# Optimization experiments

Measured on AMD Instinct MI355X. Metric: run time of the kernel, lower is better.

Reference implementation:

```python
import jax, jax.numpy as jnp
import numpy as np

NA, NS = 50000, 5000          # artist / style node counts
E_AA, E_AS = 500000, 250000   # edges per edge type
C, ED = 128, 8                # hidden dim, edge-attr dim
DIN_A, DIN_S = 128, 64        # input feature dims
NUM_LAYERS = 3


def _l2norm(x):
    # F.normalize(x, dim=-1): x / max(||x||_2, eps)
    n = jnp.sqrt(jnp.sum(x * x, axis=-1, keepdims=True))
    return x / jnp.maximum(n, 1e-12)


def _gatv2(x_src, x_dst, src, dst, eattr, Wl, Wr, att, We, b, num_dst):
    # PyG GATv2Conv, heads=1, concat=True, add_self_loops=False, edge_dim=ED
    xl = x_src @ Wl                      # [Nsrc, C] transformed source
    xr = x_dst @ Wr                      # [Ndst, C] transformed target
    m = xl[src] + xr[dst] + eattr @ We   # [E, C]
    e = jax.nn.leaky_relu(m, 0.2) @ att  # [E] attention logits
    # segment softmax over destination nodes
    emax = jax.ops.segment_max(e, dst, num_segments=num_dst)
    ee = jnp.exp(e - emax[dst])
    den = jax.ops.segment_sum(ee, dst, num_segments=num_dst)
    alpha = ee / jnp.maximum(den[dst], 1e-16)
    out = jax.ops.segment_sum(alpha[:, None] * xl[src], dst, num_segments=num_dst)
    return out + b


def setup_inputs() -> dict:
    key = jax.random.key(0)
    ks = iter(jax.random.split(key, 40))
    r = lambda shape, s=1.0: s * jax.random.normal(next(ks), shape, dtype=jnp.float32)
    d = {}
    d['x_artist'] = r((NA, DIN_A))
    d['x_style'] = r((NS, DIN_S))
    d['src_aa'] = jax.random.randint(next(ks), (E_AA,), 0, NA, dtype=jnp.int32)
    d['dst_aa'] = jax.random.randint(next(ks), (E_AA,), 0, NA, dtype=jnp.int32)
    d['eattr_aa'] = r((E_AA, ED))
    d['src_as'] = jax.random.randint(next(ks), (E_AS,), 0, NA, dtype=jnp.int32)
    d['dst_as'] = jax.random.randint(next(ks), (E_AS,), 0, NS, dtype=jnp.int32)
    d['eattr_as'] = r((E_AS, ED))
    w = 0.1
    # layer 0 (input dims differ per edge type)
    d['Wl0_aa'] = r((DIN_A, C), w); d['Wr0_aa'] = r((DIN_A, C), w)
    d['att0_aa'] = r((C,), w); d['We0_aa'] = r((ED, C), w); d['b0_aa'] = r((C,), w)
    d['Wl0_as'] = r((DIN_A, C), w); d['Wr0_as'] = r((DIN_S, C), w)
    d['att0_as'] = r((C,), w); d['We0_as'] = r((ED, C), w); d['b0_as'] = r((C,), w)
    # layers 1..2 stacked
    d['Wl_aa'] = r((2, C, C), w); d['Wr_aa'] = r((2, C, C), w)
    d['att_aa'] = r((2, C), w); d['We_aa'] = r((2, ED, C), w); d['b_aa'] = r((2, C), w)
    d['Wl_as'] = r((2, C, C), w); d['Wr_as'] = r((2, C, C), w)
    d['att_as'] = r((2, C), w); d['We_as'] = r((2, ED, C), w); d['b_as'] = r((2, C), w)
    return d


def reference(x_artist, x_style, src_aa, dst_aa, eattr_aa, src_as, dst_as, eattr_as,
              Wl0_aa, Wr0_aa, att0_aa, We0_aa, b0_aa,
              Wl0_as, Wr0_as, att0_as, We0_as, b0_as,
              Wl_aa, Wr_aa, att_aa, We_aa, b_aa,
              Wl_as, Wr_as, att_as, We_as, b_as):
    ha, hs = x_artist, x_style
    for i in range(NUM_LAYERS):
        if i == 0:
            p_aa = (Wl0_aa, Wr0_aa, att0_aa, We0_aa, b0_aa)
            p_as = (Wl0_as, Wr0_as, att0_as, We0_as, b0_as)
        else:
            j = i - 1
            p_aa = (Wl_aa[j], Wr_aa[j], att_aa[j], We_aa[j], b_aa[j])
            p_as = (Wl_as[j], Wr_as[j], att_as[j], We_as[j], b_as[j])
        # HeteroConv: each dst node type receives from exactly one edge type here
        na = _gatv2(ha, ha, src_aa, dst_aa, eattr_aa, *p_aa, NA)
        ns = _gatv2(ha, hs, src_as, dst_as, eattr_as, *p_as, NS)
        if i < NUM_LAYERS - 1:
            na = jax.nn.relu(na)
            ns = jax.nn.relu(ns)
        # dropout p=0.0 -> identity; then L2 normalize per node
        ha, hs = _l2norm(na), _l2norm(ns)
    return ha, hs
```

## Files before the change

### kernel.cpp

```cpp
#include <hip/hip_runtime.h>
#include <hip/hip_bf16.h>
#include <math.h>

#define NA 50000
#define NS 5000
#define E_AA 500000
#define E_AS 250000
#define CDIM 128
#define ED 8
#define NAPAD 50176
#define NSPAD 5120
#define SCAN_CH 2048

typedef __attribute__((ext_vector_type(8))) short bf16x8;
typedef __attribute__((ext_vector_type(4))) float f32x4;

__device__ inline short f2bf(float f) {
    __hip_bfloat16 h = __float2bfloat16(f);
    return *(short*)&h;
}
__device__ inline float bf2f(short s) {
    union { unsigned int u; float f; } cv;
    cv.u = ((unsigned int)(unsigned short)s) << 16;
    return cv.f;
}


__device__ inline float4 f4fma(float s, float4 a, float4 b) {
    return make_float4(fmaf(s, a.x, b.x), fmaf(s, a.y, b.y),
                       fmaf(s, a.z, b.z), fmaf(s, a.w, b.w));
}
__device__ inline float4 f4add(float4 a, float4 b) {
    return make_float4(a.x + b.x, a.y + b.y, a.z + b.z, a.w + b.w);
}
__device__ inline float4 f4leaky(float4 a) {
    return make_float4(a.x > 0.f ? a.x : 0.2f * a.x, a.y > 0.f ? a.y : 0.2f * a.y,
                       a.z > 0.f ? a.z : 0.2f * a.z, a.w > 0.f ? a.w : 0.2f * a.w);
}
__device__ inline float f4dot(float4 a, float4 b) {
    return a.x * b.x + a.y * b.y + a.z * b.z + a.w * b.w;
}
__device__ inline float4 f4mix(float sc, float4 a, float p, float4 x) {
    return make_float4(fmaf(sc, a.x, p * x.x), fmaf(sc, a.y, p * x.y),
                       fmaf(sc, a.z, p * x.z), fmaf(sc, a.w, p * x.w));
}
__device__ inline float4 bfh2f4(bf16x8 v, int half) {
    int o = half * 4;
    return make_float4(bf2f(v[o]), bf2f(v[o + 1]), bf2f(v[o + 2]), bf2f(v[o + 3]));
}


__global__ __launch_bounds__(256) void count2_k(const int* __restrict__ dst0,
                                                const int* __restrict__ dst1,
                                                int* __restrict__ deg0,
                                                int* __restrict__ deg1) {
    int e = blockIdx.x * 256 + threadIdx.x;
    if (e < E_AA) atomicAdd(&deg0[dst0[e]], 1);
    if (e < E_AS) atomicAdd(&deg1[dst1[e]], 1);
}

__global__ __launch_bounds__(256) void scanA_k(const int* __restrict__ deg0, int n0,
                                               const int* __restrict__ deg1, int n1,
                                               int nb0, int* __restrict__ bsum) {
    int b = blockIdx.x;
    const int* deg; int n; int lb;
    if ((int)b < nb0) { deg = deg0; n = n0; lb = b; }
    else { deg = deg1; n = n1; lb = b - nb0; }
    int t = threadIdx.x;
    int base = lb * SCAN_CH + t * 8;
    int s = 0;
    #pragma unroll
    for (int i = 0; i < 8; ++i) { int idx = base + i; s += (idx < n) ? deg[idx] : 0; }
    int lane = t & 63, w = t >> 6;
    #pragma unroll
    for (int off = 1; off < 64; off <<= 1) {
        int u = __shfl_up(s, off, 64);
        if (lane >= off) s += u;
    }
    __shared__ int ws[4];
    if (lane == 63) ws[w] = s;
    __syncthreads();
    if (t == 0) bsum[blockIdx.x] = ws[0] + ws[1] + ws[2] + ws[3];
}

__global__ void scanB_k(int* __restrict__ bsum, int nb0, int nb1) {
    int t = threadIdx.x;
    int n = nb0 + nb1;
    int v = (t < n) ? bsum[t] : 0;
    int incl = v;
    #pragma unroll
    for (int off = 1; off < 64; off <<= 1) {
        int u = __shfl_up(incl, off, 64);
        if (t >= off) incl += u;
    }
    int excl = incl - v;
    int sum0 = __shfl(incl, nb0 - 1, 64);
    if (t >= nb0) excl -= sum0;
    if (t < n) bsum[t] = excl;
}

__global__ __launch_bounds__(256) void scanC_k(const int* __restrict__ deg0, int n0,
                                               const int* __restrict__ deg1, int n1,
                                               int nb0, const int* __restrict__ bsum,
                                               int* __restrict__ rs0, int* __restrict__ rs1) {
    int b = blockIdx.x;
    const int* deg; int n; int* rs; int lb;
    if ((int)b < nb0) { deg = deg0; n = n0; rs = rs0; lb = b; }
    else { deg = deg1; n = n1; rs = rs1; lb = b - nb0; }
    int boff = bsum[b];
    int t = threadIdx.x;
    int base = lb * SCAN_CH + t * 8;
    int v[8];
    int tsum = 0;
    #pragma unroll
    for (int i = 0; i < 8; ++i) {
        int idx = base + i;
        v[i] = (idx < n) ? deg[idx] : 0;
        tsum += v[i];
    }
    int lane = t & 63, w = t >> 6;
    int incl = tsum;
    #pragma unroll
    for (int off = 1; off < 64; off <<= 1) {
        int u = __shfl_up(incl, off, 64);
        if (lane >= off) incl += u;
    }
    __shared__ int ws[4];
    if (lane == 63) ws[w] = incl;
    __syncthreads();
    int woff = 0;
    for (int i = 0; i < w; ++i) woff += ws[i];
    int run = boff + woff + incl - tsum;
    #pragma unroll
    for (int i = 0; i < 8; ++i) {
        int idx = base + i;
        if (idx < n) {
            rs[idx] = run;
            run += v[i];
            if (idx == n - 1) rs[n] = run;
        }
    }
}

__global__ __launch_bounds__(256) void scatter2_k(
    const int* __restrict__ dst0, const int* __restrict__ src0, const float* __restrict__ ea0,
    const int* __restrict__ dst1, const int* __restrict__ src1, const float* __restrict__ ea1,
    const int* __restrict__ rs0, const int* __restrict__ rs1,
    int* __restrict__ cur0, int* __restrict__ cur1,
    int* __restrict__ csrsrc0, int* __restrict__ csrsrc1,
    short* __restrict__ eas0, short* __restrict__ eas1) {
    int e = blockIdx.x * 256 + threadIdx.x;
    if (e < E_AA) {
        int d = dst0[e];
        int pos = atomicAdd(&cur0[d], 1);
        int slot = rs0[d] + pos;
        csrsrc0[slot] = src0[e];
        float4 a = ((const float4*)ea0)[(size_t)e * 2];
        float4 b = ((const float4*)ea0)[(size_t)e * 2 + 1];
        bf16x8 pk;
        pk[0] = f2bf(a.x); pk[1] = f2bf(a.y); pk[2] = f2bf(a.z); pk[3] = f2bf(a.w);
        pk[4] = f2bf(b.x); pk[5] = f2bf(b.y); pk[6] = f2bf(b.z); pk[7] = f2bf(b.w);
        *(bf16x8*)(eas0 + (size_t)slot * 8) = pk;
    }
    if (e < E_AS) {
        int d = dst1[e];
        int pos = atomicAdd(&cur1[d], 1);
        int slot = rs1[d] + pos;
        csrsrc1[slot] = src1[e];
        float4 a = ((const float4*)ea1)[(size_t)e * 2];
        float4 b = ((const float4*)ea1)[(size_t)e * 2 + 1];
        bf16x8 pk;
        pk[0] = f2bf(a.x); pk[1] = f2bf(a.y); pk[2] = f2bf(a.z); pk[3] = f2bf(a.w);
        pk[4] = f2bf(b.x); pk[5] = f2bf(b.y); pk[6] = f2bf(b.z); pk[7] = f2bf(b.w);
        *(bf16x8*)(eas1 + (size_t)slot * 8) = pk;
    }
}


__global__ __launch_bounds__(256) void deghist2_k(const int* __restrict__ rs0, int n0,
                                                  const int* __restrict__ rs1, int n1,
                                                  int nb0, int* __restrict__ dh0,
                                                  int* __restrict__ dh1) {
    int b = blockIdx.x;
    const int* rs; int n; int* dh; int lb;
    if ((int)b < nb0) { rs = rs0; n = n0; dh = dh0; lb = b; }
    else { rs = rs1; n = n1; dh = dh1; lb = b - nb0; }
    __shared__ int lh[256];
    int t = threadIdx.x;
    lh[t] = 0;
    __syncthreads();
    int d = lb * 256 + t;
    if (d < n) {
        int deg = rs[d + 1] - rs[d];
        if (deg > 255) deg = 255;
        atomicAdd(&lh[deg], 1);
    }
    __syncthreads();
    if (lh[t]) atomicAdd(&dh[t], lh[t]);
}

__global__ void binscan2_k(const int* __restrict__ dh0, const int* __restrict__ dh1,
                           int* __restrict__ dbo0, int* __restrict__ dbo1) {
    int w = threadIdx.x >> 6, lane = threadIdx.x & 63;
    const int* dh = w ? dh1 : dh0;
    int* dbo = w ? dbo1 : dbo0;
    int v[4]; int s = 0;
    #pragma unroll
    for (int i = 0; i < 4; ++i) { v[i] = dh[lane * 4 + i]; s += v[i]; }
    int incl = s;
    #pragma unroll
    for (int off = 1; off < 64; off <<= 1) {
        int u = __shfl_up(incl, off, 64);
        if (lane >= off) incl += u;
    }
    int run = incl - s;
    #pragma unroll
    for (int i = 0; i < 4; ++i) { dbo[lane * 4 + i] = run; run += v[i]; }
}

__global__ __launch_bounds__(256) void degscatter2_k(const int* __restrict__ rs0, int n0,
                                                     const int* __restrict__ rs1, int n1,
                                                     int nb0,
                                                     const int* __restrict__ dbo0,
                                                     const int* __restrict__ dbo1,
                                                     int* __restrict__ dcur0,
                                                     int* __restrict__ dcur1,
                                                     int* __restrict__ perm0,
                                                     int* __restrict__ perm1) {
    int b = blockIdx.x;
    const int* rs; int n; const int* dbo; int* dcur; int* perm; int lb;
    if ((int)b < nb0) { rs = rs0; n = n0; dbo = dbo0; dcur = dcur0; perm = perm0; lb = b; }
    else { rs = rs1; n = n1; dbo = dbo1; dcur = dcur1; perm = perm1; lb = b - nb0; }
    __shared__ int lh[256];
    __shared__ int lbase[256];
    int t = threadIdx.x;
    lh[t] = 0;
    __syncthreads();
    int d = lb * 256 + t;
    int deg = 0, lpos = 0;
    if (d < n) {
        deg = rs[d + 1] - rs[d];
        if (deg > 255) deg = 255;
        lpos = atomicAdd(&lh[deg], 1);
    }
    __syncthreads();
    int cnt = lh[t];
    if (cnt) lbase[t] = atomicAdd(&dcur[t], cnt);
    __syncthreads();
    if (d < n) perm[dbo[deg] + lbase[deg] + lpos] = d;
}


__global__ __launch_bounds__(256) void cvt2_k(const float* __restrict__ xa,
                                              const float* __restrict__ xs,
                                              short* __restrict__ Xb,
                                              short* __restrict__ Xsb) {
    const int t4A = NAPAD * 32;
    const int t4S = NSPAD * 32;
    int i = blockIdx.x * 256 + threadIdx.x;
    if (i < t4A) {
        int row = i >> 5, c4 = i & 31;
        float4 v = make_float4(0.f, 0.f, 0.f, 0.f);
        if (row < NA) v = ((const float4*)xa)[(size_t)row * 32 + c4];
        short4 s;
        s.x = f2bf(v.x); s.y = f2bf(v.y); s.z = f2bf(v.z); s.w = f2bf(v.w);
        ((short4*)Xb)[i] = s;
    } else if (i < t4A + t4S) {
        int j = i - t4A;
        int row = j >> 5, c4 = j & 31;
        float4 v = make_float4(0.f, 0.f, 0.f, 0.f);
        if (row < NS && c4 < 16) v = ((const float4*)xs)[(size_t)row * 16 + c4];
        short4 s;
        s.x = f2bf(v.x); s.y = f2bf(v.y); s.z = f2bf(v.z); s.w = f2bf(v.w);
        ((short4*)Xsb)[j] = s;
    }
}


__global__ __launch_bounds__(256) void wtr12_k(
    const float* __restrict__ Wl0_aa, const float* __restrict__ Wr0_aa,
    const float* __restrict__ Wl0_as, const float* __restrict__ Wr0_as,
    const float* __restrict__ Wl_aa, const float* __restrict__ Wr_aa,
    const float* __restrict__ Wl_as, const float* __restrict__ Wr_as,
    short* __restrict__ Wt) {
    int mat = blockIdx.x >> 6;
    int layer = mat >> 2, w = mat & 3;
    int idx = (blockIdx.x & 63) * 256 + threadIdx.x;
    int k = idx >> 7, n = idx & 127;
    const float* W;
    int K = 128;
    if (layer == 0) {
        W = (w == 0) ? Wl0_aa : (w == 1) ? Wr0_aa : (w == 2) ? Wl0_as : Wr0_as;
        if (w == 3) K = 64;
    } else {
        int j = layer - 1;
        W = ((w == 0) ? Wl_aa : (w == 1) ? Wr_aa : (w == 2) ? Wl_as : Wr_as)
            + (size_t)j * 16384;
    }
    float v = (k < K) ? W[(size_t)k * 128 + n] : 0.f;
    Wt[(size_t)mat * 16384 + n * 128 + k] = f2bf(v);
}


__global__ __launch_bounds__(256) void gemm4_k(
    const short* __restrict__ Xb, const short* __restrict__ Xsb,
    const short* __restrict__ Wt,
    short* __restrict__ Y0b, short* __restrict__ Y1b, short* __restrict__ Y2b,
    short* __restrict__ Y3b, int gM) {
    int t = threadIdx.x;
    int wave = t >> 6, lane = t & 63;
    int quad = lane >> 4, l16 = lane & 15;
    bool style = (int)blockIdx.x >= gM;
    int rblk = style ? (int)blockIdx.x - gM : (int)blockIdx.x;
    const short* X = style ? Xsb : Xb;
    int rbase = rblk * 256 + wave * 64;

    bf16x8 a[4][4];
    #pragma unroll
    for (int rt = 0; rt < 4; ++rt) {
        const short* arow = X + (size_t)(rbase + rt * 16 + l16) * 128 + quad * 8;
        #pragma unroll
        for (int kb = 0; kb < 4; ++kb) a[rt][kb] = *(const bf16x8*)(arow + kb * 32);
    }

    if (!style) {
        short* Yp[3] = {Y0b, Y1b, Y2b};
        #pragma unroll
        for (int w = 0; w < 3; ++w) {
            const short* Wb = Wt + (size_t)w * 16384;
            #pragma unroll 2
            for (int nt = 0; nt < 8; ++nt) {
                const short* brow = Wb + (size_t)(nt * 16 + l16) * 128 + quad * 8;
                bf16x8 b[4];
                #pragma unroll
                for (int kb = 0; kb < 4; ++kb) b[kb] = *(const bf16x8*)(brow + kb * 32);
                f32x4 acc[4] = {{0,0,0,0},{0,0,0,0},{0,0,0,0},{0,0,0,0}};
                #pragma unroll
                for (int kb = 0; kb < 4; ++kb)
                    #pragma unroll
                    for (int rt = 0; rt < 4; ++rt)
                        acc[rt] = __builtin_amdgcn_mfma_f32_16x16x32_bf16(a[rt][kb], b[kb],
                                                                          acc[rt], 0, 0, 0);
                int col = nt * 16 + l16;
                #pragma unroll
                for (int rt = 0; rt < 4; ++rt) {
                    #pragma unroll
                    for (int r = 0; r < 4; ++r) {
                        int row = rbase + rt * 16 + quad * 4 + r;
                        if (row < NA) Yp[w][(size_t)row * 128 + col] = f2bf(acc[rt][r]);
                    }
                }
            }
        }
    } else {
        const short* Wb = Wt + (size_t)3 * 16384;
        #pragma unroll 2
        for (int nt = 0; nt < 8; ++nt) {
            const short* brow = Wb + (size_t)(nt * 16 + l16) * 128 + quad * 8;
            bf16x8 b[4];
            #pragma unroll
            for (int kb = 0; kb < 4; ++kb) b[kb] = *(const bf16x8*)(brow + kb * 32);
            f32x4 acc[4] = {{0,0,0,0},{0,0,0,0},{0,0,0,0},{0,0,0,0}};
            #pragma unroll
            for (int kb = 0; kb < 4; ++kb)
                #pragma unroll
                for (int rt = 0; rt < 4; ++rt)
                    acc[rt] = __builtin_amdgcn_mfma_f32_16x16x32_bf16(a[rt][kb], b[kb],
                                                                      acc[rt], 0, 0, 0);
            int col = nt * 16 + l16;
            #pragma unroll
            for (int rt = 0; rt < 4; ++rt) {
                #pragma unroll
                for (int r = 0; r < 4; ++r) {
                    int row = rbase + rt * 16 + quad * 4 + r;
                    if (row < NS) Y3b[(size_t)row * 128 + col] = f2bf(acc[rt][r]);
                }
            }
        }
    }
}


template<bool RELU>
__global__ __launch_bounds__(256, 2) void agg2_k(
    const short* __restrict__ xl0, const short* __restrict__ xr0,
    const short* __restrict__ eas0, const int* __restrict__ csrsrc0,
    const float* __restrict__ We0, const float* __restrict__ att0,
    const float* __restrict__ bias0, const int* __restrict__ rs0,
    const int* __restrict__ perm0,
    float* __restrict__ out0, short* __restrict__ outb0, int nd0, int nblk0,
    const short* __restrict__ xl1, const short* __restrict__ xr1,
    const short* __restrict__ eas1, const int* __restrict__ csrsrc1,
    const float* __restrict__ We1, const float* __restrict__ att1,
    const float* __restrict__ bias1, const int* __restrict__ rs1,
    const int* __restrict__ perm1,
    float* __restrict__ out1, short* __restrict__ outb1, int nd1) {

    const short* xl; const short* xrp; const short* eas; const int* csrsrc;
    const float* We; const float* att; const float* bias;
    const int* row_start; const int* perm;
    float* out; short* outb; int ndst, blk;
    if ((int)blockIdx.x < nblk0) {
        xl = xl0; xrp = xr0; eas = eas0; csrsrc = csrsrc0; We = We0; att = att0; bias = bias0;
        row_start = rs0; perm = perm0; out = out0; outb = outb0;
        ndst = nd0; blk = blockIdx.x;
    } else {
        xl = xl1; xrp = xr1; eas = eas1; csrsrc = csrsrc1; We = We1; att = att1; bias = bias1;
        row_start = rs1; perm = perm1; out = out1; outb = outb1;
        ndst = nd1; blk = blockIdx.x - nblk0;
    }

    int wave = threadIdx.x >> 6;
    int lane = threadIdx.x & 63;
    int g = lane >> 4;
    int sl = lane & 15;
    int c = sl * 8;

    int di = blk * 16 + wave * 4 + g;
    bool has = di < ndst;
    int d = has ? perm[ndst - 1 - di] : 0;

    float4 WeA[8], WeB[8];
    #pragma unroll
    for (int k = 0; k < 8; ++k) {
        WeA[k] = *(const float4*)(We + k * 128 + c);
        WeB[k] = *(const float4*)(We + k * 128 + c + 4);
    }
    float4 attA = *(const float4*)(att + c);
    float4 attB = *(const float4*)(att + c + 4);
    bf16x8 xrb = *(const bf16x8*)(xrp + (size_t)d * 128 + c);
    float4 xrA = bfh2f4(xrb, 0), xrB = bfh2f4(xrb, 1);

    #pragma unroll
    for (int k = 0; k < 8; ++k) {
        asm volatile("" : "+v"(WeA[k].x), "+v"(WeA[k].y), "+v"(WeA[k].z), "+v"(WeA[k].w));
        asm volatile("" : "+v"(WeB[k].x), "+v"(WeB[k].y), "+v"(WeB[k].z), "+v"(WeB[k].w));
    }
    asm volatile("" : "+v"(attA.x), "+v"(attA.y), "+v"(attA.z), "+v"(attA.w));
    asm volatile("" : "+v"(attB.x), "+v"(attB.y), "+v"(attB.z), "+v"(attB.w));
    asm volatile("" : "+v"(xrA.x), "+v"(xrA.y), "+v"(xrA.z), "+v"(xrA.w));
    asm volatile("" : "+v"(xrB.x), "+v"(xrB.y), "+v"(xrB.z), "+v"(xrB.w));

    float4 accA = {0,0,0,0}, accB = {0,0,0,0};
    float den = 0.f, mrun = -INFINITY;

    int e0 = has ? row_start[d] : 0;
    int cnt = has ? row_start[d + 1] - e0 : 0;
    int last = (cnt > 0) ? e0 + cnt - 1 : 0;

    int mc = cnt;
    mc = max(mc, __shfl_xor(mc, 16, 64));
    mc = max(mc, __shfl_xor(mc, 32, 64));
    int niter = (mc + 3) >> 2;

    auto lds_idx = [&](int ib, int* s) {
        #pragma unroll
        for (int j = 0; j < 4; ++j) {
            int cj = (ib + j < last) ? ib + j : last;
            s[j] = csrsrc[cj];
        }
    };
    auto lds_ea = [&](int ib, bf16x8* ea) {
        #pragma unroll
        for (int j = 0; j < 4; ++j) {
            int cj = (ib + j < last) ? ib + j : last;
            ea[j] = *(const bf16x8*)(eas + (size_t)cj * 8);
        }
    };
    auto lds_x = [&](const int* s, bf16x8* xb) {
        #pragma unroll
        for (int j = 0; j < 4; ++j)
            xb[j] = *(const bf16x8*)(xl + (size_t)s[j] * 128 + c);
    };

    int sA[4], sB[4];
    bf16x8 xbA[4], xbB[4], eaA[4], eaB[4];

    if (niter > 0) {
        int st[4];
        lds_idx(e0, st);
        lds_ea(e0, eaA);
        lds_x(st, xbA);
        lds_idx(e0 + 4, sA);
    }

    auto step = [&](int i, bf16x8 (&xbC)[4], bf16x8 (&eaC)[4], int (&sNx)[4],
                    bf16x8 (&xbN)[4], bf16x8 (&eaN)[4], int (&sN2)[4]) {
        lds_x(sNx, xbN);
        lds_ea(e0 + i + 4, eaN);
        lds_idx(e0 + i + 8, sN2);

        float4 x0A = bfh2f4(xbC[0], 0), x0B = bfh2f4(xbC[0], 1);
        float4 x1A = bfh2f4(xbC[1], 0), x1B = bfh2f4(xbC[1], 1);
        float4 x2A = bfh2f4(xbC[2], 0), x2B = bfh2f4(xbC[2], 1);
        float4 x3A = bfh2f4(xbC[3], 0), x3B = bfh2f4(xbC[3], 1);

        auto logit = [&](float4 xA, float4 xB, bf16x8 eab) -> float {
            float4 ea = bfh2f4(eab, 0), eb = bfh2f4(eab, 1);
            float4 mA = f4add(xA, xrA), mB = f4add(xB, xrB);
            mA = f4fma(ea.x, WeA[0], mA); mB = f4fma(ea.x, WeB[0], mB);
            mA = f4fma(ea.y, WeA[1], mA); mB = f4fma(ea.y, WeB[1], mB);
            mA = f4fma(ea.z, WeA[2], mA); mB = f4fma(ea.z, WeB[2], mB);
            mA = f4fma(ea.w, WeA[3], mA); mB = f4fma(ea.w, WeB[3], mB);
            mA = f4fma(eb.x, WeA[4], mA); mB = f4fma(eb.x, WeB[4], mB);
            mA = f4fma(eb.y, WeA[5], mA); mB = f4fma(eb.y, WeB[5], mB);
            mA = f4fma(eb.z, WeA[6], mA); mB = f4fma(eb.z, WeB[6], mB);
            mA = f4fma(eb.w, WeA[7], mA); mB = f4fma(eb.w, WeB[7], mB);
            return f4dot(f4leaky(mA), attA) + f4dot(f4leaky(mB), attB);
        };

        float t0 = logit(x0A, x0B, eaC[0]);
        float t1 = logit(x1A, x1B, eaC[1]);
        float t2 = logit(x2A, x2B, eaC[2]);
        float t3 = logit(x3A, x3B, eaC[3]);
        #pragma unroll
        for (int off = 8; off; off >>= 1) {
            t0 += __shfl_xor(t0, off, 64);
            t1 += __shfl_xor(t1, off, 64);
            t2 += __shfl_xor(t2, off, 64);
            t3 += __shfl_xor(t3, off, 64);
        }
        if (i + 1 >= cnt) t1 = -INFINITY;
        if (i + 2 >= cnt) t2 = -INFINITY;
        if (i + 3 >= cnt) t3 = -INFINITY;

        if (i < cnt) {
            float m4 = fmaxf(fmaxf(t0, t1), fmaxf(t2, t3));
            float nm = fmaxf(mrun, m4);
            float sc = __expf(mrun - nm);
            float p0 = __expf(t0 - nm);
            float p1 = __expf(t1 - nm);
            float p2 = __expf(t2 - nm);
            float p3 = __expf(t3 - nm);
            den = den * sc + p0 + p1 + p2 + p3;
            accA = f4mix(sc, accA, p0, x0A);
            accA = f4fma(p1, x1A, accA);
            accA = f4fma(p2, x2A, accA);
            accA = f4fma(p3, x3A, accA);
            accB = f4mix(sc, accB, p0, x0B);
            accB = f4fma(p1, x1B, accB);
            accB = f4fma(p2, x2B, accB);
            accB = f4fma(p3, x3B, accB);
            mrun = nm;
        }
    };

    int it = 0;
    for (; it + 1 < niter; it += 2) {
        step(it * 4,     xbA, eaA, sA, xbB, eaB, sB);
        step(it * 4 + 4, xbB, eaB, sB, xbA, eaA, sA);
    }
    if (it < niter)
        step(it * 4, xbA, eaA, sA, xbB, eaB, sB);

    float4 bA = *(const float4*)(bias + c);
    float4 bB = *(const float4*)(bias + c + 4);

    float inv = 1.f / fmaxf(den, 1e-16f);
    float4 oA = make_float4(accA.x * inv + bA.x, accA.y * inv + bA.y,
                            accA.z * inv + bA.z, accA.w * inv + bA.w);
    float4 oB = make_float4(accB.x * inv + bB.x, accB.y * inv + bB.y,
                            accB.z * inv + bB.z, accB.w * inv + bB.w);
    if (RELU) {
        oA = make_float4(fmaxf(oA.x,0.f), fmaxf(oA.y,0.f), fmaxf(oA.z,0.f), fmaxf(oA.w,0.f));
        oB = make_float4(fmaxf(oB.x,0.f), fmaxf(oB.y,0.f), fmaxf(oB.z,0.f), fmaxf(oB.w,0.f));
    }
    float ss = f4dot(oA, oA) + f4dot(oB, oB);
    #pragma unroll
    for (int off = 8; off; off >>= 1) ss += __shfl_xor(ss, off, 64);
    float innv = 1.f / fmaxf(sqrtf(ss), 1e-12f);
    oA = make_float4(oA.x * innv, oA.y * innv, oA.z * innv, oA.w * innv);
    oB = make_float4(oB.x * innv, oB.y * innv, oB.z * innv, oB.w * innv);
    if (has) {
        if (out) {
            float4* op = (float4*)(out + (size_t)d * 128 + c);
            op[0] = oA;
            op[1] = oB;
        }
        if (outb) {
            bf16x8 pk;
            pk[0] = f2bf(oA.x); pk[1] = f2bf(oA.y); pk[2] = f2bf(oA.z); pk[3] = f2bf(oA.w);
            pk[4] = f2bf(oB.x); pk[5] = f2bf(oB.y); pk[6] = f2bf(oB.z); pk[7] = f2bf(oB.w);
            *(bf16x8*)(outb + (size_t)d * 128 + c) = pk;
        }
    }
}


extern "C" void kernel_launch(void* const* d_in, const int* in_sizes, int n_in,
                              void* d_out, int out_size, void* d_ws, size_t ws_size,
                              hipStream_t stream) {
    const float* x_artist = (const float*)d_in[0];
    const float* x_style  = (const float*)d_in[1];
    const int*   src_aa   = (const int*)d_in[2];
    const int*   dst_aa   = (const int*)d_in[3];
    const float* eattr_aa = (const float*)d_in[4];
    const int*   src_as   = (const int*)d_in[5];
    const int*   dst_as   = (const int*)d_in[6];
    const float* eattr_as = (const float*)d_in[7];
    const float* Wl0_aa = (const float*)d_in[8];
    const float* Wr0_aa = (const float*)d_in[9];
    const float* att0_aa = (const float*)d_in[10];
    const float* We0_aa = (const float*)d_in[11];
    const float* b0_aa = (const float*)d_in[12];
    const float* Wl0_as = (const float*)d_in[13];
    const float* Wr0_as = (const float*)d_in[14];
    const float* att0_as = (const float*)d_in[15];
    const float* We0_as = (const float*)d_in[16];
    const float* b0_as = (const float*)d_in[17];
    const float* Wl_aa = (const float*)d_in[18];
    const float* Wr_aa = (const float*)d_in[19];
    const float* att_aa = (const float*)d_in[20];
    const float* We_aa = (const float*)d_in[21];
    const float* b_aa = (const float*)d_in[22];
    const float* Wl_as = (const float*)d_in[23];
    const float* Wr_as = (const float*)d_in[24];
    const float* att_as = (const float*)d_in[25];
    const float* We_as = (const float*)d_in[26];
    const float* b_as = (const float*)d_in[27];

    float* out = (float*)d_out;

    short* Xb    = (short*)d_ws;
    short* Xsb   = Xb + (size_t)NAPAD * 128;
    short* Wt    = Xsb + (size_t)NSPAD * 128;
    short* bufAb = Wt + 12 * 16384;
    short* bufDb = bufAb + (size_t)NA * 128;
    short* bufBb = bufDb + (size_t)NA * 128;
    short* bufCb = bufBb + (size_t)NA * 128;
    short* easAA = bufCb + (size_t)NSPAD * 128;
    short* easAS = easAA + (size_t)E_AA * 8;
    int* ip = (int*)(easAS + (size_t)E_AS * 8);
    int* zbase  = ip;
    int* deg_aa = ip;            ip += NA;
    int* cur_aa = ip;            ip += NA;
    int* deg_as = ip;            ip += NS;
    int* cur_as = ip;            ip += NS;
    int* dh_aa  = ip;            ip += 256;
    int* dh_as  = ip;            ip += 256;
    int* dcur_aa = ip;           ip += 256;
    int* dcur_as = ip;           ip += 256;
    size_t zbytes = (size_t)(ip - zbase) * sizeof(int);
    int* rs_aa  = ip;            ip += NA + 1;
    int* rs_as  = ip;            ip += NS + 1;
    int* csrsrc_aa = ip;         ip += E_AA;
    int* csrsrc_as = ip;         ip += E_AS;
    int* perm_aa = ip;           ip += NA;
    int* perm_as = ip;           ip += NS;
    int* dbo_aa = ip;            ip += 256;
    int* dbo_as = ip;            ip += 256;
    int* bsum   = ip;            ip += 64;

    const int nbA_scan = (NA + SCAN_CH - 1) / SCAN_CH;
    const int nbS_scan = (NS + SCAN_CH - 1) / SCAN_CH;
    const int nbA_node = (NA + 255) / 256;
    const int nbS_node = (NS + 255) / 256;
    const int gE = (E_AA + 255) / 256;

    hipMemsetAsync(zbase, 0, zbytes, stream);
    count2_k<<<gE, 256, 0, stream>>>(dst_aa, dst_as, deg_aa, deg_as);
    scanA_k<<<nbA_scan + nbS_scan, 256, 0, stream>>>(deg_aa, NA, deg_as, NS, nbA_scan, bsum);
    scanB_k<<<1, 64, 0, stream>>>(bsum, nbA_scan, nbS_scan);
    scanC_k<<<nbA_scan + nbS_scan, 256, 0, stream>>>(deg_aa, NA, deg_as, NS, nbA_scan,
                                                     bsum, rs_aa, rs_as);
    scatter2_k<<<gE, 256, 0, stream>>>(dst_aa, src_aa, eattr_aa,
                                       dst_as, src_as, eattr_as,
                                       rs_aa, rs_as, cur_aa, cur_as,
                                       csrsrc_aa, csrsrc_as, easAA, easAS);
    deghist2_k<<<nbA_node + nbS_node, 256, 0, stream>>>(rs_aa, NA, rs_as, NS, nbA_node,
                                                        dh_aa, dh_as);
    binscan2_k<<<1, 128, 0, stream>>>(dh_aa, dh_as, dbo_aa, dbo_as);
    degscatter2_k<<<nbA_node + nbS_node, 256, 0, stream>>>(rs_aa, NA, rs_as, NS, nbA_node,
                                                           dbo_aa, dbo_as, dcur_aa, dcur_as,
                                                           perm_aa, perm_as);
    cvt2_k<<<(NAPAD * 32 + NSPAD * 32 + 255) / 256, 256, 0, stream>>>(x_artist, x_style,
                                                                      Xb, Xsb);
    wtr12_k<<<12 * 64, 256, 0, stream>>>(Wl0_aa, Wr0_aa, Wl0_as, Wr0_as,
                                         Wl_aa, Wr_aa, Wl_as, Wr_as, Wt);

    const int gM = NAPAD / 256;
    const int gS4 = NSPAD / 256;
    const int aggA = (NA + 15) / 16;
    const int aggS = (NS + 15) / 16;

    for (int layer = 0; layer < 3; ++layer) {
        int j = layer - 1;
        const float *patt_aa, *pWe_aa, *pb_aa, *patt_as, *pWe_as, *pb_as;
        if (layer == 0) {
            patt_aa = att0_aa; pWe_aa = We0_aa; pb_aa = b0_aa;
            patt_as = att0_as; pWe_as = We0_as; pb_as = b0_as;
        } else {
            patt_aa = att_aa + (size_t)j * CDIM;
            pWe_aa = We_aa + (size_t)j * ED * CDIM;
            pb_aa = b_aa + (size_t)j * CDIM;
            patt_as = att_as + (size_t)j * CDIM;
            pWe_as = We_as + (size_t)j * ED * CDIM;
            pb_as = b_as + (size_t)j * CDIM;
        }
        const short* pWt = Wt + (size_t)layer * 4 * 16384;
        float* hA_out = (layer == 2) ? out : nullptr;
        float* hS_out = (layer == 2) ? out + (size_t)NA * CDIM : nullptr;
        short* hA_outb = (layer == 2) ? nullptr : Xb;
        short* hS_outb = (layer == 2) ? nullptr : Xsb;

        gemm4_k<<<gM + gS4, 256, 0, stream>>>(Xb, Xsb, pWt, bufAb, bufBb, bufDb, bufCb, gM);

        if (layer < 2)
            agg2_k<true><<<aggA + aggS, 256, 0, stream>>>(
                bufAb, bufBb, easAA, csrsrc_aa, pWe_aa, patt_aa, pb_aa,
                rs_aa, perm_aa, hA_out, hA_outb, NA, aggA,
                bufDb, bufCb, easAS, csrsrc_as, pWe_as, patt_as, pb_as,
                rs_as, perm_as, hS_out, hS_outb, NS);
        else
            agg2_k<false><<<aggA + aggS, 256, 0, stream>>>(
                bufAb, bufBb, easAA, csrsrc_aa, pWe_aa, patt_aa, pb_aa,
                rs_aa, perm_aa, hA_out, hA_outb, NA, aggA,
                bufDb, bufCb, easAS, csrsrc_as, pWe_as, patt_as, pb_as,
                rs_as, perm_as, hS_out, hS_outb, NS);
    }
}
```

Baseline: 552.6 us.

## Make aggregation kernel persistent with packed job descriptors and prefetched next job

The aggregation kernel becomes a persistent grid of fixed size that loops over destination-node tiles, first for artist and then for style destinations. Weights, attention and bias are loaded once per segment instead of once per tile. The degree-sorting step now writes int4 job records (node, edge start, degree), which removes the perm and row_start lookups from the aggregation path. The next job and its xr row are prefetched during the current tile. The aim is to cut block launch and setup overhead and dependent index loads, at the cost of a fixed grid that may balance load worse and a larger job array.

```diff
diff --git a/kernel.cpp b/kernel.cpp
--- a/kernel.cpp
+++ b/kernel.cpp
@@ -11,6 +11,7 @@
 #define NAPAD 50176
 #define NSPAD 5120
 #define SCAN_CH 2048
+#define AGG_BLOCKS 1024
 
 typedef __attribute__((ext_vector_type(8))) short bf16x8;
 typedef __attribute__((ext_vector_type(4))) float f32x4;
@@ -225,29 +226,30 @@
                                                      const int* __restrict__ dbo1,
                                                      int* __restrict__ dcur0,
                                                      int* __restrict__ dcur1,
-                                                     int* __restrict__ perm0,
-                                                     int* __restrict__ perm1) {
+                                                     int4* __restrict__ jobs0,
+                                                     int4* __restrict__ jobs1) {
     int b = blockIdx.x;
-    const int* rs; int n; const int* dbo; int* dcur; int* perm; int lb;
-    if ((int)b < nb0) { rs = rs0; n = n0; dbo = dbo0; dcur = dcur0; perm = perm0; lb = b; }
-    else { rs = rs1; n = n1; dbo = dbo1; dcur = dcur1; perm = perm1; lb = b - nb0; }
+    const int* rs; int n; const int* dbo; int* dcur; int4* jobs; int lb;
+    if ((int)b < nb0) { rs = rs0; n = n0; dbo = dbo0; dcur = dcur0; jobs = jobs0; lb = b; }
+    else { rs = rs1; n = n1; dbo = dbo1; dcur = dcur1; jobs = jobs1; lb = b - nb0; }
     __shared__ int lh[256];
     __shared__ int lbase[256];
     int t = threadIdx.x;
     lh[t] = 0;
     __syncthreads();
     int d = lb * 256 + t;
-    int deg = 0, lpos = 0;
+    int deg = 0, lpos = 0, e0 = 0, degc = 0;
     if (d < n) {
-        deg = rs[d + 1] - rs[d];
-        if (deg > 255) deg = 255;
-        lpos = atomicAdd(&lh[deg], 1);
+        e0 = rs[d];
+        deg = rs[d + 1] - e0;
+        degc = deg > 255 ? 255 : deg;
+        lpos = atomicAdd(&lh[degc], 1);
     }
     __syncthreads();
     int cnt = lh[t];
     if (cnt) lbase[t] = atomicAdd(&dcur[t], cnt);
     __syncthreads();
-    if (d < n) perm[dbo[deg] + lbase[deg] + lpos] = d;
+    if (d < n) jobs[dbo[degc] + lbase[degc] + lpos] = make_int4(d, e0, deg, 0);
 }
 
 
@@ -386,202 +388,219 @@
     const short* __restrict__ xl0, const short* __restrict__ xr0,
     const short* __restrict__ eas0, const int* __restrict__ csrsrc0,
     const float* __restrict__ We0, const float* __restrict__ att0,
-    const float* __restrict__ bias0, const int* __restrict__ rs0,
-    const int* __restrict__ perm0,
+    const float* __restrict__ bias0, const int4* __restrict__ jobs0,
     float* __restrict__ out0, short* __restrict__ outb0, int nd0, int nblk0,
     const short* __restrict__ xl1, const short* __restrict__ xr1,
     const short* __restrict__ eas1, const int* __restrict__ csrsrc1,
     const float* __restrict__ We1, const float* __restrict__ att1,
-    const float* __restrict__ bias1, const int* __restrict__ rs1,
-    const int* __restrict__ perm1,
-    float* __restrict__ out1, short* __restrict__ outb1, int nd1) {
-
-    const short* xl; const short* xrp; const short* eas; const int* csrsrc;
-    const float* We; const float* att; const float* bias;
-    const int* row_start; const int* perm;
-    float* out; short* outb; int ndst, blk;
-    if ((int)blockIdx.x < nblk0) {
-        xl = xl0; xrp = xr0; eas = eas0; csrsrc = csrsrc0; We = We0; att = att0; bias = bias0;
-        row_start = rs0; perm = perm0; out = out0; outb = outb0;
-        ndst = nd0; blk = blockIdx.x;
-    } else {
-        xl = xl1; xrp = xr1; eas = eas1; csrsrc = csrsrc1; We = We1; att = att1; bias = bias1;
-        row_start = rs1; perm = perm1; out = out1; outb = outb1;
-        ndst = nd1; blk = blockIdx.x - nblk0;
-    }
+    const float* __restrict__ bias1, const int4* __restrict__ jobs1,
+    float* __restrict__ out1, short* __restrict__ outb1, int nd1, int nblk1) {
 
     int wave = threadIdx.x >> 6;
     int lane = threadIdx.x & 63;
     int g = lane >> 4;
     int sl = lane & 15;
     int c = sl * 8;
-
-    int di = blk * 16 + wave * 4 + g;
-    bool has = di < ndst;
-    int d = has ? perm[ndst - 1 - di] : 0;
-
-    float4 WeA[8], WeB[8];
-    #pragma unroll
-    for (int k = 0; k < 8; ++k) {
-        WeA[k] = *(const float4*)(We + k * 128 + c);
-        WeB[k] = *(const float4*)(We + k * 128 + c + 4);
-    }
-    float4 attA = *(const float4*)(att + c);
-    float4 attB = *(const float4*)(att + c + 4);
-    bf16x8 xrb = *(const bf16x8*)(xrp + (size_t)d * 128 + c);
-    float4 xrA = bfh2f4(xrb, 0), xrB = bfh2f4(xrb, 1);
-
-    #pragma unroll
-    for (int k = 0; k < 8; ++k) {
-        asm volatile("" : "+v"(WeA[k].x), "+v"(WeA[k].y), "+v"(WeA[k].z), "+v"(WeA[k].w));
-        asm volatile("" : "+v"(WeB[k].x), "+v"(WeB[k].y), "+v"(WeB[k].z), "+v"(WeB[k].w));
-    }
-    asm volatile("" : "+v"(attA.x), "+v"(attA.y), "+v"(attA.z), "+v"(attA.w));
-    asm volatile("" : "+v"(attB.x), "+v"(attB.y), "+v"(attB.z), "+v"(attB.w));
-    asm volatile("" : "+v"(xrA.x), "+v"(xrA.y), "+v"(xrA.z), "+v"(xrA.w));
-    asm volatile("" : "+v"(xrB.x), "+v"(xrB.y), "+v"(xrB.z), "+v"(xrB.w));
-
-    float4 accA = {0,0,0,0}, accB = {0,0,0,0};
-    float den = 0.f, mrun = -INFINITY;
-
-    int e0 = has ? row_start[d] : 0;
-    int cnt = has ? row_start[d + 1] - e0 : 0;
-    int last = (cnt > 0) ? e0 + cnt - 1 : 0;
-
-    int mc = cnt;
-    mc = max(mc, __shfl_xor(mc, 16, 64));
-    mc = max(mc, __shfl_xor(mc, 32, 64));
-    int niter = (mc + 3) >> 2;
-
-    auto lds_idx = [&](int ib, int* s) {
+    int stride = gridDim.x;
+
+    for (int seg = 0; seg < 2; ++seg) {
+        const short* xl = seg ? xl1 : xl0;
+        const short* xrp = seg ? xr1 : xr0;
+        const short* eas = seg ? eas1 : eas0;
+        const int* csrsrc = seg ? csrsrc1 : csrsrc0;
+        const float* We = seg ? We1 : We0;
+        const float* att = seg ? att1 : att0;
+        const float* bias = seg ? bias1 : bias0;
+        const int4* jobs = seg ? jobs1 : jobs0;
+        float* out = seg ? out1 : out0;
+        short* outb = seg ? outb1 : outb0;
+        int ndst = seg ? nd1 : nd0;
+        int nblk = seg ? nblk1 : nblk0;
+
+        int blk = blockIdx.x;
+        if (blk >= nblk) continue;
+
+        float4 WeA[8], WeB[8];
         #pragma unroll
-        for (int j = 0; j < 4; ++j) {
-            int cj = (ib + j < last) ? ib + j : last;
-            s[j] = csrsrc[cj];
+        for (int k = 0; k < 8; ++k) {
+            WeA[k] = *(const float4*)(We + k * 128 + c);
+            WeB[k] = *(const float4*)(We + k * 128 + c + 4);
         }
-    };
-    auto lds_ea = [&](int ib, bf16x8* ea) {
+        float4 attA = *(const float4*)(att + c);
+        float4 attB = *(const float4*)(att + c + 4);
+        float4 bA = *(const float4*)(bias + c);
+        float4 bB = *(const float4*)(bias + c + 4);
         #pragma unroll
-        for (int j = 0; j < 4; ++j) {
-            int cj = (ib + j < last) ? ib + j : last;
-            ea[j] = *(const bf16x8*)(eas + (size_t)cj * 8);
+        for (int k = 0; k < 8; ++k) {
+            asm volatile("" : "+v"(WeA[k].x), "+v"(WeA[k].y), "+v"(WeA[k].z), "+v"(WeA[k].w));
+            asm volatile("" : "+v"(WeB[k].x), "+v"(WeB[k].y), "+v"(WeB[k].z), "+v"(WeB[k].w));
         }
-    };
-    auto lds_x = [&](const int* s, bf16x8* xb) {
-        #pragma unroll
-        for (int j = 0; j < 4; ++j)
-            xb[j] = *(const bf16x8*)(xl + (size_t)s[j] * 128 + c);
-    };
-
-    int sA[4], sB[4];
-    bf16x8 xbA[4], xbB[4], eaA[4], eaB[4];
-
-    if (niter > 0) {
-        int st[4];
-        lds_idx(e0, st);
-        lds_ea(e0, eaA);
-        lds_x(st, xbA);
-        lds_idx(e0 + 4, sA);
-    }
-
-    auto step = [&](int i, bf16x8 (&xbC)[4], bf16x8 (&eaC)[4], int (&sNx)[4],
-                    bf16x8 (&xbN)[4], bf16x8 (&eaN)[4], int (&sN2)[4]) {
-        lds_x(sNx, xbN);
-        lds_ea(e0 + i + 4, eaN);
-        lds_idx(e0 + i + 8, sN2);
-
-        float4 x0A = bfh2f4(xbC[0], 0), x0B = bfh2f4(xbC[0], 1);
-        float4 x1A = bfh2f4(xbC[1], 0), x1B = bfh2f4(xbC[1], 1);
-        float4 x2A = bfh2f4(xbC[2], 0), x2B = bfh2f4(xbC[2], 1);
-        float4 x3A = bfh2f4(xbC[3], 0), x3B = bfh2f4(xbC[3], 1);
-
-        auto logit = [&](float4 xA, float4 xB, bf16x8 eab) -> float {
-            float4 ea = bfh2f4(eab, 0), eb = bfh2f4(eab, 1);
-            float4 mA = f4add(xA, xrA), mB = f4add(xB, xrB);
-            mA = f4fma(ea.x, WeA[0], mA); mB = f4fma(ea.x, WeB[0], mB);
-            mA = f4fma(ea.y, WeA[1], mA); mB = f4fma(ea.y, WeB[1], mB);
-            mA = f4fma(ea.z, WeA[2], mA); mB = f4fma(ea.z, WeB[2], mB);
-            mA = f4fma(ea.w, WeA[3], mA); mB = f4fma(ea.w, WeB[3], mB);
-            mA = f4fma(eb.x, WeA[4], mA); mB = f4fma(eb.x, WeB[4], mB);
-            mA = f4fma(eb.y, WeA[5], mA); mB = f4fma(eb.y, WeB[5], mB);
-            mA = f4fma(eb.z, WeA[6], mA); mB = f4fma(eb.z, WeB[6], mB);
-            mA = f4fma(eb.w, WeA[7], mA); mB = f4fma(eb.w, WeB[7], mB);
-            return f4dot(f4leaky(mA), attA) + f4dot(f4leaky(mB), attB);
+        asm volatile("" : "+v"(attA.x), "+v"(attA.y), "+v"(attA.z), "+v"(attA.w));
+        asm volatile("" : "+v"(attB.x), "+v"(attB.y), "+v"(attB.z), "+v"(attB.w));
+
+        auto load_job = [&](int b) -> int4 {
+            int di = b * 16 + wave * 4 + g;
+            bool h = di < ndst;
+            int4 j = jobs[h ? (ndst - 1 - di) : 0];
+            if (!h) j.z = 0;
+            return j;
         };
 
-        float t0 = logit(x0A, x0B, eaC[0]);
-        float t1 = logit(x1A, x1B, eaC[1]);
-        float t2 = logit(x2A, x2B, eaC[2]);
-        float t3 = logit(x3A, x3B, eaC[3]);
-        #pragma unroll
-        for (int off = 8; off; off >>= 1) {
-            t0 += __shfl_xor(t0, off, 64);
-            t1 += __shfl_xor(t1, off, 64);
-            t2 += __shfl_xor(t2, off, 64);
-            t3 += __shfl_xor(t3, off, 64);
-        }
-        if (i + 1 >= cnt) t1 = -INFINITY;
-        if (i + 2 >= cnt) t2 = -INFINITY;
-        if (i + 3 >= cnt) t3 = -INFINITY;
-
-        if (i < cnt) {
-            float m4 = fmaxf(fmaxf(t0, t1), fmaxf(t2, t3));
-            float nm = fmaxf(mrun, m4);
-            float sc = __expf(mrun - nm);
-            float p0 = __expf(t0 - nm);
-            float p1 = __expf(t1 - nm);
-            float p2 = __expf(t2 - nm);
-            float p3 = __expf(t3 - nm);
-            den = den * sc + p0 + p1 + p2 + p3;
-            accA = f4mix(sc, accA, p0, x0A);
-            accA = f4fma(p1, x1A, accA);
-            accA = f4fma(p2, x2A, accA);
-            accA = f4fma(p3, x3A, accA);
-            accB = f4mix(sc, accB, p0, x0B);
-            accB = f4fma(p1, x1B, accB);
-            accB = f4fma(p2, x2B, accB);
-            accB = f4fma(p3, x3B, accB);
-            mrun = nm;
-        }
-    };
-
-    int it = 0;
-    for (; it + 1 < niter; it += 2) {
-        step(it * 4,     xbA, eaA, sA, xbB, eaB, sB);
-        step(it * 4 + 4, xbB, eaB, sB, xbA, eaA, sA);
-    }
-    if (it < niter)
-        step(it * 4, xbA, eaA, sA, xbB, eaB, sB);
-
-    float4 bA = *(const float4*)(bias + c);
-    float4 bB = *(const float4*)(bias + c + 4);
-
-    float inv = 1.f / fmaxf(den, 1e-16f);
-    float4 oA = make_float4(accA.x * inv + bA.x, accA.y * inv + bA.y,
-                            accA.z * inv + bA.z, accA.w * inv + bA.w);
-    float4 oB = make_float4(accB.x * inv + bB.x, accB.y * inv + bB.y,
-                            accB.z * inv + bB.z, accB.w * inv + bB.w);
-    if (RELU) {
-        oA = make_float4(fmaxf(oA.x,0.f), fmaxf(oA.y,0.f), fmaxf(oA.z,0.f), fmaxf(oA.w,0.f));
-        oB = make_float4(fmaxf(oB.x,0.f), fmaxf(oB.y,0.f), fmaxf(oB.z,0.f), fmaxf(oB.w,0.f));
-    }
-    float ss = f4dot(oA, oA) + f4dot(oB, oB);
-    #pragma unroll
-    for (int off = 8; off; off >>= 1) ss += __shfl_xor(ss, off, 64);
-    float innv = 1.f / fmaxf(sqrtf(ss), 1e-12f);
-    oA = make_float4(oA.x * innv, oA.y * innv, oA.z * innv, oA.w * innv);
-    oB = make_float4(oB.x * innv, oB.y * innv, oB.z * innv, oB.w * innv);
-    if (has) {
-        if (out) {
-            float4* op = (float4*)(out + (size_t)d * 128 + c);
-            op[0] = oA;
-            op[1] = oB;
-        }
-        if (outb) {
-            bf16x8 pk;
-            pk[0] = f2bf(oA.x); pk[1] = f2bf(oA.y); pk[2] = f2bf(oA.z); pk[3] = f2bf(oA.w);
-            pk[4] = f2bf(oB.x); pk[5] = f2bf(oB.y); pk[6] = f2bf(oB.z); pk[7] = f2bf(oB.w);
-            *(bf16x8*)(outb + (size_t)d * 128 + c) = pk;
+        int4 jb = load_job(blk);
+        bf16x8 xrb = *(const bf16x8*)(xrp + (size_t)jb.x * 128 + c);
+
+        for (; blk < nblk; blk += stride) {
+            int nb = blk + stride;
+            int4 jbN = (nb < nblk) ? load_job(nb) : make_int4(0, 0, 0, 0);
+
+            int d = jb.x, e0 = jb.y, cnt = jb.z;
+            int di = blk * 16 + wave * 4 + g;
+            bool has = di < ndst;
+            float4 xrA = bfh2f4(xrb, 0), xrB = bfh2f4(xrb, 1);
+
+            float4 accA = {0,0,0,0}, accB = {0,0,0,0};
+            float den = 0.f, mrun = -INFINITY;
+            int last = (cnt > 0) ? e0 + cnt - 1 : 0;
+
+            int mc = cnt;
+            mc = max(mc, __shfl_xor(mc, 16, 64));
+            mc = max(mc, __shfl_xor(mc, 32, 64));
+            int niter = (mc + 3) >> 2;
+
+            auto lds_idx = [&](int ib, int* s) {
+                #pragma unroll
+                for (int j = 0; j < 4; ++j) {
+                    int cj = (ib + j < last) ? ib + j : last;
+                    s[j] = csrsrc[cj];
+                }
+            };
+            auto lds_ea = [&](int ib, bf16x8* ea) {
+                #pragma unroll
+                for (int j = 0; j < 4; ++j) {
+                    int cj = (ib + j < last) ? ib + j : last;
+                    ea[j] = *(const bf16x8*)(eas + (size_t)cj * 8);
+                }
+            };
+            auto lds_x = [&](const int* s, bf16x8* xb) {
+                #pragma unroll
+                for (int j = 0; j < 4; ++j)
+                    xb[j] = *(const bf16x8*)(xl + (size_t)s[j] * 128 + c);
+            };
+
+            int sA[4], sB[4];
+            bf16x8 xbA[4], xbB[4], eaA[4], eaB[4];
+
+            if (niter > 0) {
+                int st[4];
+                lds_idx(e0, st);
+                lds_ea(e0, eaA);
+                lds_x(st, xbA);
+                lds_idx(e0 + 4, sA);
+            }
+
+            auto step = [&](int i, bf16x8 (&xbC)[4], bf16x8 (&eaC)[4], int (&sNx)[4],
+                            bf16x8 (&xbN)[4], bf16x8 (&eaN)[4], int (&sN2)[4]) {
+                lds_x(sNx, xbN);
+                lds_ea(e0 + i + 4, eaN);
+                lds_idx(e0 + i + 8, sN2);
+
+                float4 x0A = bfh2f4(xbC[0], 0), x0B = bfh2f4(xbC[0], 1);
+                float4 x1A = bfh2f4(xbC[1], 0), x1B = bfh2f4(xbC[1], 1);
+                float4 x2A = bfh2f4(xbC[2], 0), x2B = bfh2f4(xbC[2], 1);
+                float4 x3A = bfh2f4(xbC[3], 0), x3B = bfh2f4(xbC[3], 1);
+
+                auto logit = [&](float4 xA, float4 xB, bf16x8 eab) -> float {
+                    float4 ea = bfh2f4(eab, 0), eb = bfh2f4(eab, 1);
+                    float4 mA = f4add(xA, xrA), mB = f4add(xB, xrB);
+                    mA = f4fma(ea.x, WeA[0], mA); mB = f4fma(ea.x, WeB[0], mB);
+                    mA = f4fma(ea.y, WeA[1], mA); mB = f4fma(ea.y, WeB[1], mB);
+                    mA = f4fma(ea.z, WeA[2], mA); mB = f4fma(ea.z, WeB[2], mB);
+                    mA = f4fma(ea.w, WeA[3], mA); mB = f4fma(ea.w, WeB[3], mB);
+                    mA = f4fma(eb.x, WeA[4], mA); mB = f4fma(eb.x, WeB[4], mB);
+                    mA = f4fma(eb.y, WeA[5], mA); mB = f4fma(eb.y, WeB[5], mB);
+                    mA = f4fma(eb.z, WeA[6], mA); mB = f4fma(eb.z, WeB[6], mB);
+                    mA = f4fma(eb.w, WeA[7], mA); mB = f4fma(eb.w, WeB[7], mB);
+                    return f4dot(f4leaky(mA), attA) + f4dot(f4leaky(mB), attB);
+                };
+
+                float t0 = logit(x0A, x0B, eaC[0]);
+                float t1 = logit(x1A, x1B, eaC[1]);
+                float t2 = logit(x2A, x2B, eaC[2]);
+                float t3 = logit(x3A, x3B, eaC[3]);
+                #pragma unroll
+                for (int off = 8; off; off >>= 1) {
+                    t0 += __shfl_xor(t0, off, 64);
+                    t1 += __shfl_xor(t1, off, 64);
+                    t2 += __shfl_xor(t2, off, 64);
+                    t3 += __shfl_xor(t3, off, 64);
+                }
+                if (i + 1 >= cnt) t1 = -INFINITY;
+                if (i + 2 >= cnt) t2 = -INFINITY;
+                if (i + 3 >= cnt) t3 = -INFINITY;
+
+                if (i < cnt) {
+                    float m4 = fmaxf(fmaxf(t0, t1), fmaxf(t2, t3));
+                    float nm = fmaxf(mrun, m4);
+                    float sc = __expf(mrun - nm);
+                    float p0 = __expf(t0 - nm);
+                    float p1 = __expf(t1 - nm);
+                    float p2 = __expf(t2 - nm);
+                    float p3 = __expf(t3 - nm);
+                    den = den * sc + p0 + p1 + p2 + p3;
+                    accA = f4mix(sc, accA, p0, x0A);
+                    accA = f4fma(p1, x1A, accA);
+                    accA = f4fma(p2, x2A, accA);
+                    accA = f4fma(p3, x3A, accA);
+                    accB = f4mix(sc, accB, p0, x0B);
+                    accB = f4fma(p1, x1B, accB);
+                    accB = f4fma(p2, x2B, accB);
+                    accB = f4fma(p3, x3B, accB);
+                    mrun = nm;
+                }
+            };
+
+            int it = 0;
+            for (; it + 1 < niter; it += 2) {
+                step(it * 4,     xbA, eaA, sA, xbB, eaB, sB);
+                step(it * 4 + 4, xbB, eaB, sB, xbA, eaA, sA);
+            }
+            if (it < niter)
+                step(it * 4, xbA, eaA, sA, xbB, eaB, sB);
+
+            float inv = 1.f / fmaxf(den, 1e-16f);
+            float4 oA = make_float4(accA.x * inv + bA.x, accA.y * inv + bA.y,
+                                    accA.z * inv + bA.z, accA.w * inv + bA.w);
+            float4 oB = make_float4(accB.x * inv + bB.x, accB.y * inv + bB.y,
+                                    accB.z * inv + bB.z, accB.w * inv + bB.w);
+            if (RELU) {
+                oA = make_float4(fmaxf(oA.x,0.f), fmaxf(oA.y,0.f),
+                                 fmaxf(oA.z,0.f), fmaxf(oA.w,0.f));
+                oB = make_float4(fmaxf(oB.x,0.f), fmaxf(oB.y,0.f),
+                                 fmaxf(oB.z,0.f), fmaxf(oB.w,0.f));
+            }
+            float ss = f4dot(oA, oA) + f4dot(oB, oB);
+            #pragma unroll
+            for (int off = 8; off; off >>= 1) ss += __shfl_xor(ss, off, 64);
+            float innv = 1.f / fmaxf(sqrtf(ss), 1e-12f);
+            oA = make_float4(oA.x * innv, oA.y * innv, oA.z * innv, oA.w * innv);
+            oB = make_float4(oB.x * innv, oB.y * innv, oB.z * innv, oB.w * innv);
+            if (has) {
+                if (out) {
+                    float4* op = (float4*)(out + (size_t)d * 128 + c);
+                    op[0] = oA;
+                    op[1] = oB;
+                }
+                if (outb) {
+                    bf16x8 pk;
+                    pk[0] = f2bf(oA.x); pk[1] = f2bf(oA.y); pk[2] = f2bf(oA.z); pk[3] = f2bf(oA.w);
+                    pk[4] = f2bf(oB.x); pk[5] = f2bf(oB.y); pk[6] = f2bf(oB.z); pk[7] = f2bf(oB.w);
+                    *(bf16x8*)(outb + (size_t)d * 128 + c) = pk;
+                }
+            }
+
+            bf16x8 xrbN = *(const bf16x8*)(xrp + (size_t)jbN.x * 128 + c);
+            jb = jbN;
+            xrb = xrbN;
         }
     }
 }
@@ -641,12 +660,12 @@
     int* dcur_aa = ip;           ip += 256;
     int* dcur_as = ip;           ip += 256;
     size_t zbytes = (size_t)(ip - zbase) * sizeof(int);
+    int4* jobs_aa = (int4*)ip;   ip += 4 * NA;
+    int4* jobs_as = (int4*)ip;   ip += 4 * NS;
     int* rs_aa  = ip;            ip += NA + 1;
     int* rs_as  = ip;            ip += NS + 1;
     int* csrsrc_aa = ip;         ip += E_AA;
     int* csrsrc_as = ip;         ip += E_AS;
-    int* perm_aa = ip;           ip += NA;
-    int* perm_as = ip;           ip += NS;
     int* dbo_aa = ip;            ip += 256;
     int* dbo_as = ip;            ip += 256;
     int* bsum   = ip;            ip += 64;
@@ -672,7 +691,7 @@
     binscan2_k<<<1, 128, 0, stream>>>(dh_aa, dh_as, dbo_aa, dbo_as);
     degscatter2_k<<<nbA_node + nbS_node, 256, 0, stream>>>(rs_aa, NA, rs_as, NS, nbA_node,
                                                            dbo_aa, dbo_as, dcur_aa, dcur_as,
-                                                           perm_aa, perm_as);
+                                                           jobs_aa, jobs_as);
     cvt2_k<<<(NAPAD * 32 + NSPAD * 32 + 255) / 256, 256, 0, stream>>>(x_artist, x_style,
                                                                       Xb, Xsb);
     wtr12_k<<<12 * 64, 256, 0, stream>>>(Wl0_aa, Wr0_aa, Wl0_as, Wr0_as,
@@ -706,16 +725,16 @@
         gemm4_k<<<gM + gS4, 256, 0, stream>>>(Xb, Xsb, pWt, bufAb, bufBb, bufDb, bufCb, gM);
 
         if (layer < 2)
-            agg2_k<true><<<aggA + aggS, 256, 0, stream>>>(
+            agg2_k<true><<<AGG_BLOCKS, 256, 0, stream>>>(
                 bufAb, bufBb, easAA, csrsrc_aa, pWe_aa, patt_aa, pb_aa,
-                rs_aa, perm_aa, hA_out, hA_outb, NA, aggA,
+                jobs_aa, hA_out, hA_outb, NA, aggA,
                 bufDb, bufCb, easAS, csrsrc_as, pWe_as, patt_as, pb_as,
-                rs_as, perm_as, hS_out, hS_outb, NS);
+                jobs_as, hS_out, hS_outb, NS, aggS);
         else
-            agg2_k<false><<<aggA + aggS, 256, 0, stream>>>(
+            agg2_k<false><<<AGG_BLOCKS, 256, 0, stream>>>(
                 bufAb, bufBb, easAA, csrsrc_aa, pWe_aa, patt_aa, pb_aa,
-                rs_aa, perm_aa, hA_out, hA_outb, NA, aggA,
+                jobs_aa, hA_out, hA_outb, NA, aggA,
                 bufDb, bufCb, easAS, csrsrc_as, pWe_as, patt_as, pb_as,
-                rs_as, perm_as, hS_out, hS_outb, NS);
-    }
-}
+                jobs_as, hS_out, hS_outb, NS, aggS);
+    }
+}
```

Measured after the change: 535.2 us. 1.03x faster.
